# Performance work log

Measured on AMD Instinct MI355X. Metric: run time of the kernel, lower is better.

Reference implementation:

```python
import jax, jax.numpy as jnp
import numpy as np

D_FEAT = 6
T = 60
H = 64          # hidden_size
N = 8192        # number of stocks (cross-sectional batch)
LRELU_SLOPE = 0.01
BN_EPS = 1e-5


def _gru_layer(x_seq, W_ih, W_hh, b_ih, b_hh):
    """torch-convention GRU layer. x_seq: (N, T, in) -> (N, T, H)."""
    # precompute input projections for all timesteps: (N, T, 3H)
    xw = jnp.einsum('nti,gi->ntg', x_seq, W_ih) + b_ih

    def step(h, xt):
        gh = h @ W_hh.T + b_hh
        xr, xz, xn = jnp.split(xt, 3, axis=-1)
        hr, hz, hn = jnp.split(gh, 3, axis=-1)
        r = jax.nn.sigmoid(xr + hr)
        z = jax.nn.sigmoid(xz + hz)
        n = jnp.tanh(xn + r * hn)
        h_new = (1.0 - z) * n + z * h
        return h_new, h_new

    h0 = jnp.zeros((x_seq.shape[0], H), x_seq.dtype)
    _, ys = jax.lax.scan(step, h0, jnp.swapaxes(xw, 0, 1))  # (T, N, H)
    return jnp.swapaxes(ys, 0, 1)


def _batchnorm(x, w, b):
    # track_running_stats=False -> always batch statistics (biased var)
    m = jnp.mean(x, axis=0)
    v = jnp.var(x, axis=0)
    return (x - m) * jax.lax.rsqrt(v + BN_EPS) * w + b


def setup_inputs() -> dict:
    key = jax.random.key(0)
    ks = jax.random.split(key, 24)
    s = 1.0 / np.sqrt(H)

    def u(k, shape):
        return jax.random.uniform(k, shape, jnp.float32, -s, s)

    inp = {"x": jax.random.normal(ks[0], (N, D_FEAT * T), jnp.float32)}
    in_sizes = [D_FEAT, H]
    for l in range(2):
        inp[f"W_ih_l{l}"] = u(ks[1 + 4 * l], (3 * H, in_sizes[l]))
        inp[f"W_hh_l{l}"] = u(ks[2 + 4 * l], (3 * H, H))
        inp[f"b_ih_l{l}"] = u(ks[3 + 4 * l], (3 * H,))
        inp[f"b_hh_l{l}"] = u(ks[4 + 4 * l], (3 * H,))
    inp["bn1_w"] = 1.0 + 0.1 * jax.random.normal(ks[9], (H,), jnp.float32)
    inp["bn1_b"] = 0.1 * jax.random.normal(ks[10], (H,), jnp.float32)
    inp["fc_w"] = u(ks[11], (H, H))
    inp["fc_b"] = u(ks[12], (H,))
    inp["bn2_w"] = 1.0 + 0.1 * jax.random.normal(ks[13], (H,), jnp.float32)
    inp["bn2_b"] = 0.1 * jax.random.normal(ks[14], (H,), jnp.float32)
    inp["fc_out_w"] = u(ks[15], (1, H))
    inp["fc_out_b"] = u(ks[16], (1,))
    return inp


def reference(x, W_ih_l0, W_hh_l0, b_ih_l0, b_hh_l0,
              W_ih_l1, W_hh_l1, b_ih_l1, b_hh_l1,
              bn1_w, bn1_b, fc_w, fc_b, bn2_w, bn2_b, fc_out_w, fc_out_b):
    n = x.shape[0]
    xs = x.reshape(n, D_FEAT, -1).transpose(0, 2, 1)  # (N, T, d_feat)
    h = _gru_layer(xs, W_ih_l0, W_hh_l0, b_ih_l0, b_hh_l0)
    h = _gru_layer(h, W_ih_l1, W_hh_l1, b_ih_l1, b_hh_l1)
    hidden = h[:, -1, :]                               # (N, H)
    hidden = _batchnorm(hidden, bn1_w, bn1_b)

    # pairwise covariance: E[x_i * y_j] - E[x_i]E[y_j], mean over H.
    # Algebraically (x @ y.T)/H - e_x e_y^T; no O(N^2*H) intermediate.
    e = jnp.mean(hidden, axis=1, keepdims=True)        # (N, 1)
    gamma = hidden @ hidden.T / H - e @ e.T            # (N, N)

    out = gamma @ hidden                               # (N, H)
    out = out @ fc_w.T + fc_b
    out = _batchnorm(out, bn2_w, bn2_b)
    out = jnp.where(out >= 0, out, LRELU_SLOPE * out)  # LeakyReLU(0.01)
    return (out @ fc_out_w.T + fc_out_b).squeeze()
```

## Files before the change

kernel.cpp:

```cpp
#include <hip/hip_runtime.h>
#include <hip/hip_bf16.h>
#include <hip/hip_cooperative_groups.h>

namespace cg = cooperative_groups;

#define N_ROWS 8192
#define T_STEPS 60
#define DFEAT 6

typedef _Float16 f16x8 __attribute__((ext_vector_type(8)));
typedef float f32x4 __attribute__((ext_vector_type(4)));
typedef float fvec4 __attribute__((ext_vector_type(4)));

#if __has_builtin(__builtin_amdgcn_exp2f)
#define EXP2F(x) __builtin_amdgcn_exp2f(x)
#else
#define EXP2F(x) exp2f(x)
#endif
#define RCPF(x) __builtin_amdgcn_rcpf(x)

#define LOG2E  1.4426950408889634f
#define LOG2E2 2.8853900817779268f

#define MFMA16(a, b, c) __builtin_amdgcn_mfma_f32_16x16x32_f16(a, b, c, 0, 0, 0)

#define LOAD_WS(W, g, kf, SC, DST) do {                                       \
    const float* _p = (W) + ((g)*64 + jcol)*64 + (kf)*32 + rowgrp*8;          \
    fvec4 _v0 = *(const fvec4*)_p;                                            \
    fvec4 _v1 = *(const fvec4*)(_p + 4);                                      \
    f16x8 _f;                                                                 \
    _Pragma("unroll")                                                         \
    for (int _e = 0; _e < 4; ++_e) {                                          \
        _f[_e]     = (_Float16)(_v0[_e] * (SC));                              \
        _f[4 + _e] = (_Float16)(_v1[_e] * (SC));                              \
    }                                                                         \
    DST = _f;                                                                 \
} while (0)

__device__ __forceinline__ int hswz(int row, int col) {
    return row * 64 + (col ^ ((row & 7) << 3));
}

__global__ __launch_bounds__(512, 4)
void gru_fused(const float* __restrict__ x,
               const float* __restrict__ Wih0, const float* __restrict__ Whh0,
               const float* __restrict__ bih0, const float* __restrict__ bhh0,
               const float* __restrict__ Wih1, const float* __restrict__ Whh1,
               const float* __restrict__ bih1, const float* __restrict__ bhh1,
               float* __restrict__ hidden)
{
    __shared__ __align__(16) _Float16 h0s[2][1024];
    __shared__ __align__(16) _Float16 h1s[2][1024];
    __shared__ __align__(16) _Float16 xs[T_STEPS][16][8];
    __shared__ __align__(16) _Float16 zx[8];

    const int tid = threadIdx.x;
    const int lane = tid & 63;
    const int wv = tid >> 6;
    const int roleB = wv >> 2;
    const int cg_ = wv & 3;
    const int lrow = lane & 15;
    const int rowgrp = lane >> 4;
    const int jcol = cg_ * 16 + lrow;
    const int rbase = blockIdx.x * 16;

    for (int i = tid; i < 1024; i += 512) {
        h0s[0][i] = (_Float16)0.f; h0s[1][i] = (_Float16)0.f;
        h1s[0][i] = (_Float16)0.f; h1s[1][i] = (_Float16)0.f;
    }
    if (tid < 8) zx[tid] = (_Float16)0.f;
    for (int idx = tid; idx < 16 * T_STEPS; idx += 512) {
        int t = idx >> 4, r = idx & 15;
        const float* xp = x + (long)(rbase + r) * (DFEAT * T_STEPS) + t;
        f16x8 f;
#pragma unroll
        for (int d = 0; d < DFEAT; ++d) f[d] = (_Float16)xp[d * T_STEPS];
        f[6] = (_Float16)0.f; f[7] = (_Float16)0.f;
        *(f16x8*)&xs[t][r][0] = f;
    }

    f16x8 zerof;
#pragma unroll
    for (int e = 0; e < 8; ++e) zerof[e] = (_Float16)0.f;

    f16x8 wg[12];
#pragma unroll
    for (int i = 0; i < 12; ++i) wg[i] = zerof;
    float br, bz, bxn, bhn;
    if (roleB == 0) {
        LOAD_WS(Whh0, 0, 0, LOG2E,  wg[0]);  LOAD_WS(Whh0, 0, 1, LOG2E,  wg[1]);
        LOAD_WS(Whh0, 1, 0, LOG2E,  wg[2]);  LOAD_WS(Whh0, 1, 1, LOG2E,  wg[3]);
        LOAD_WS(Whh0, 2, 0, LOG2E2, wg[4]);  LOAD_WS(Whh0, 2, 1, LOG2E2, wg[5]);
        if (rowgrp == 0) {
#pragma unroll
            for (int g = 0; g < 3; ++g) {
                const float sc = (g == 2) ? LOG2E2 : LOG2E;
                f16x8 f = zerof;
#pragma unroll
                for (int e = 0; e < DFEAT; ++e)
                    f[e] = (_Float16)(Wih0[(g * 64 + jcol) * DFEAT + e] * sc);
                wg[6 + g] = f;
            }
        }
        br  = (bih0[jcol] + bhh0[jcol]) * LOG2E;
        bz  = (bih0[64 + jcol] + bhh0[64 + jcol]) * LOG2E;
        bxn = bih0[128 + jcol] * LOG2E2;
        bhn = bhh0[128 + jcol] * LOG2E2;
    } else {
        LOAD_WS(Wih1, 0, 0, LOG2E,  wg[0]);  LOAD_WS(Wih1, 0, 1, LOG2E,  wg[1]);
        LOAD_WS(Wih1, 1, 0, LOG2E,  wg[2]);  LOAD_WS(Wih1, 1, 1, LOG2E,  wg[3]);
        LOAD_WS(Wih1, 2, 0, LOG2E2, wg[4]);  LOAD_WS(Wih1, 2, 1, LOG2E2, wg[5]);
        LOAD_WS(Whh1, 0, 0, LOG2E,  wg[6]);  LOAD_WS(Whh1, 0, 1, LOG2E,  wg[7]);
        LOAD_WS(Whh1, 1, 0, LOG2E,  wg[8]);  LOAD_WS(Whh1, 1, 1, LOG2E,  wg[9]);
        LOAD_WS(Whh1, 2, 0, LOG2E2, wg[10]); LOAD_WS(Whh1, 2, 1, LOG2E2, wg[11]);
        br  = (bih1[jcol] + bhh1[jcol]) * LOG2E;
        bz  = (bih1[64 + jcol] + bhh1[64 + jcol]) * LOG2E;
        bxn = bih1[128 + jcol] * LOG2E2;
        bhn = bhh1[128 + jcol] * LOG2E2;
    }

    float hreg[4] = {0.f, 0.f, 0.f, 0.f};

    const _Float16* xbase_l = (rowgrp == 0) ? &xs[0][lrow][0] : &zx[0];
    const long xinc = (rowgrp == 0) ? 128 : 0;

    int widx[4];
#pragma unroll
    for (int q = 0; q < 4; ++q) widx[q] = hswz(rowgrp * 4 + q, jcol);
    const int ridx0 = lrow * 64 + ((rowgrp * 8) ^ ((lrow & 7) << 3));
    const int ridx1 = lrow * 64 + ((32 + rowgrp * 8) ^ ((lrow & 7) << 3));

    __syncthreads();

#pragma unroll 1
    for (int tt = 0; tt <= T_STEPS; ++tt) {
        if (roleB == 0) {
            if (tt < T_STEPS) {
                const int rb = (tt + 1) & 1;
                f16x8 hf0 = *(const f16x8*)&h0s[rb][ridx0];
                f16x8 hf1 = *(const f16x8*)&h0s[rb][ridx1];
                f16x8 xf  = *(const f16x8*)(xbase_l + (long)tt * xinc);
                f32x4 accr  = {br, br, br, br};
                f32x4 accz  = {bz, bz, bz, bz};
                f32x4 accxn = {bxn, bxn, bxn, bxn};
                f32x4 acchn = {bhn, bhn, bhn, bhn};
                accr  = MFMA16(xf,  wg[6], accr);
                accr  = MFMA16(hf0, wg[0], accr);
                accr  = MFMA16(hf1, wg[1], accr);
                accz  = MFMA16(xf,  wg[7], accz);
                accz  = MFMA16(hf0, wg[2], accz);
                accz  = MFMA16(hf1, wg[3], accz);
                accxn = MFMA16(xf,  wg[8], accxn);
                acchn = MFMA16(hf0, wg[4], acchn);
                acchn = MFMA16(hf1, wg[5], acchn);
#pragma unroll
                for (int q = 0; q < 4; ++q) {
                    float r = RCPF(1.0f + EXP2F(-accr[q]));
                    float z = RCPF(1.0f + EXP2F(-accz[q]));
                    float v = accxn[q] + r * acchn[q];
                    float n = 2.0f * RCPF(1.0f + EXP2F(-v)) - 1.0f;
                    hreg[q] = n + z * (hreg[q] - n);
                }
                const int wb = tt & 1;
#pragma unroll
                for (int q = 0; q < 4; ++q)
                    h0s[wb][widx[q]] = (_Float16)hreg[q];
            }
        } else {
            if (tt > 0) {
                const int rb0 = (tt + 1) & 1;
                const int rb1 = tt & 1;
                f16x8 xf0 = *(const f16x8*)&h0s[rb0][ridx0];
                f16x8 xf1 = *(const f16x8*)&h0s[rb0][ridx1];
                f16x8 hf0 = *(const f16x8*)&h1s[rb1][ridx0];
                f16x8 hf1 = *(const f16x8*)&h1s[rb1][ridx1];
                f32x4 accr  = {br, br, br, br};
                f32x4 accz  = {bz, bz, bz, bz};
                f32x4 accxn = {bxn, bxn, bxn, bxn};
                f32x4 acchn = {bhn, bhn, bhn, bhn};
                accr  = MFMA16(xf0, wg[0], accr);
                accr  = MFMA16(xf1, wg[1], accr);
                accr  = MFMA16(hf0, wg[6], accr);
                accr  = MFMA16(hf1, wg[7], accr);
                accz  = MFMA16(xf0, wg[2], accz);
                accz  = MFMA16(xf1, wg[3], accz);
                accz  = MFMA16(hf0, wg[8], accz);
                accz  = MFMA16(hf1, wg[9], accz);
                accxn = MFMA16(xf0, wg[4], accxn);
                accxn = MFMA16(xf1, wg[5], accxn);
                acchn = MFMA16(hf0, wg[10], acchn);
                acchn = MFMA16(hf1, wg[11], acchn);
#pragma unroll
                for (int q = 0; q < 4; ++q) {
                    float r = RCPF(1.0f + EXP2F(-accr[q]));
                    float z = RCPF(1.0f + EXP2F(-accz[q]));
                    float v = accxn[q] + r * acchn[q];
                    float n = 2.0f * RCPF(1.0f + EXP2F(-v)) - 1.0f;
                    hreg[q] = n + z * (hreg[q] - n);
                }
                const int wb = (tt + 1) & 1;
#pragma unroll
                for (int q = 0; q < 4; ++q)
                    h1s[wb][widx[q]] = (_Float16)hreg[q];
            }
        }
        __syncthreads();
    }

    if (roleB == 1) {
#pragma unroll
        for (int q = 0; q < 4; ++q)
            hidden[(long)(rbase + rowgrp * 4 + q) * 64 + jcol] = hreg[q];
    }
}

__global__ __launch_bounds__(256, 1)
void tail_kernel(const float* __restrict__ hidden,
                 const float* __restrict__ bn1w, const float* __restrict__ bn1b,
                 const float* __restrict__ fcw,  const float* __restrict__ fcb,
                 const float* __restrict__ bn2w, const float* __restrict__ bn2b,
                 const float* __restrict__ fow,  const float* __restrict__ fob,
                 float* __restrict__ y, float* wsb)
{
    float* csp    = wsb;
    float* cqp    = wsb + 4096;
    float* spart  = wsb + 8192;
    float* e2part = wsb + 12288;
    float* sred   = wsb + 12352;
    float* E2g    = wsb + 12416;
    float* Ag     = wsb + 12480;
    float* Bg     = wsb + 12544;
    float* bMg    = wsb + 12608;
    float* svg    = wsb + 12672;
    float* Mg     = wsb + 12736;
    float* Gpart  = wsb + 16832;

    __shared__ float tile[128][65];
    __shared__ float el[128];
    __shared__ float Fs[64][65];
    __shared__ float Msh[64][65];
    __shared__ float a1s[64], c1s[64], a2s[64], c2s[64];
    __shared__ float svs[64], fcs[64], wos[64];
    __shared__ float Grow[64];
    __shared__ float r4a[4][64], r4b[4][64];

    const int b = blockIdx.x, tid = threadIdx.x;
    cg::grid_group grid = cg::this_grid();

    for (int i = tid; i < 8192; i += 256)
        tile[i >> 6][i & 63] = hidden[b * 8192 + i];
    for (int i = tid; i < 4096; i += 256)
        Fs[i >> 6][i & 63] = fcw[i];
    __syncthreads();
    {
        const int c = tid & 63, g = tid >> 6;
        float s = 0.f, q = 0.f;
        for (int r = g * 32; r < g * 32 + 32; ++r) {
            float v = tile[r][c]; s += v; q += v * v;
        }
        r4a[g][c] = s; r4b[g][c] = q;
    }
    __syncthreads();
    if (tid < 64) {
        csp[b * 64 + tid] = r4a[0][tid] + r4a[1][tid] + r4a[2][tid] + r4a[3][tid];
        cqp[b * 64 + tid] = r4b[0][tid] + r4b[1][tid] + r4b[2][tid] + r4b[3][tid];
    }
    __threadfence();
    grid.sync();

    if (tid < 64) {
        float s = 0.f, q = 0.f;
        for (int bb = 0; bb < 64; ++bb) { s += csp[bb * 64 + tid]; q += cqp[bb * 64 + tid]; }
        float m = s * (1.0f / N_ROWS);
        float v = q * (1.0f / N_ROWS) - m * m;
        float a = bn1w[tid] * rsqrtf(v + 1e-5f);
        a1s[tid] = a; c1s[tid] = bn1b[tid] - m * a;
    }
    __syncthreads();
    for (int i = tid; i < 8192; i += 256) {
        int r = i >> 6, c = i & 63;
        tile[r][c] = tile[r][c] * a1s[c] + c1s[c];
    }
    __syncthreads();
    for (int r = tid; r < 128; r += 256) {
        float s = 0.f;
#pragma unroll 8
        for (int c = 0; c < 64; ++c) s += tile[r][c];
        el[r] = s * (1.0f / 64.0f);
    }
    __syncthreads();
    {
        const int j = tid & 63, kg = tid >> 6;
        float accG[16];
#pragma unroll
        for (int q = 0; q < 16; ++q) accG[q] = 0.f;
        for (int r = 0; r < 128; ++r) {
            float hj = tile[r][j];
#pragma unroll
            for (int q = 0; q < 16; ++q) accG[q] += tile[r][kg * 16 + q] * hj;
        }
#pragma unroll
        for (int q = 0; q < 16; ++q)
            Gpart[(b * 64 + kg * 16 + q) * 64 + j] = accG[q];
    }
    if (tid < 64) {
        float accS = 0.f;
        for (int r = 0; r < 128; ++r) accS += el[r] * tile[r][tid];
        spart[b * 64 + tid] = accS;
        float p = el[tid] * el[tid] + el[tid + 64] * el[tid + 64];
#pragma unroll
        for (int o = 32; o > 0; o >>= 1) p += __shfl_down(p, o);
        if (tid == 0) e2part[b] = p;
    }
    __threadfence();
    grid.sync();

    {
        const int j = tid & 63, g = tid >> 6;
        float p = 0.f;
        for (int bb = g * 16; bb < g * 16 + 16; ++bb)
            p += Gpart[(bb * 64 + b) * 64 + j];
        r4a[g][j] = p;
    }
    __syncthreads();
    if (tid < 64)
        Grow[tid] = r4a[0][tid] + r4a[1][tid] + r4a[2][tid] + r4a[3][tid];
    __syncthreads();
    if (tid < 64) {
        const int p = tid;
        float acc = 0.f;
#pragma unroll 8
        for (int j = 0; j < 64; ++j) acc += Grow[j] * Fs[p][j];
        Mg[b * 64 + p] = acc * (1.0f / 64.0f);
    }
    if (b == 0 && tid < 64) {
        float s = 0.f;
        for (int bb = 0; bb < 64; ++bb) s += spart[bb * 64 + tid];
        sred[tid] = s;
    }
    if (b == 1 && tid < 64) { Ag[tid] = 0.f; Bg[tid] = 0.f; bMg[tid] = 0.f; }
    if (b == 2 && tid == 0) {
        float e = 0.f;
        for (int bb = 0; bb < 64; ++bb) e += e2part[bb];
        E2g[0] = e;
    }
    __threadfence();
    grid.sync();

    for (int i = tid; i < 4096; i += 256)
        Msh[i >> 6][i & 63] = Mg[i];
    __syncthreads();
    if (tid < 64) {
        const int p = tid;
        float gm = 0.f;
#pragma unroll 8
        for (int kk = 0; kk < 64; ++kk) gm += Grow[kk] * Msh[kk][p];
        float mkp = Msh[b][p];
        atomicAdd(&Ag[p],  mkp * gm);
        atomicAdd(&Bg[p],  sred[b] * mkp);
        atomicAdd(&bMg[p], bn1b[b] * mkp);
    }
    if (b == 0 && tid < 64) {
        const int p = tid;
        float sv = 0.f;
#pragma unroll 8
        for (int j = 0; j < 64; ++j) sv += sred[j] * Fs[p][j];
        svg[p] = sv;
    }
    __threadfence();
    grid.sync();

    if (tid < 64) {
        const int p = tid;
        float bsum = 0.f;
        for (int j = 0; j < 64; ++j) bsum += bn1b[j];
        float Esum = (float)N_ROWS * bsum * (1.0f / 64.0f);
        float svp = svg[p];
        float Su  = (float)N_ROWS * bMg[p] - Esum * svp;
        float Su2 = Ag[p] - 2.0f * svp * Bg[p] + E2g[0] * svp * svp;
        float f = fcb[p];
        float cs = Su + (float)N_ROWS * f;
        float cq = Su2 + 2.0f * f * Su + (float)N_ROWS * f * f;
        float m2 = cs * (1.0f / N_ROWS);
        float v2 = cq * (1.0f / N_ROWS) - m2 * m2;
        float a = bn2w[p] * rsqrtf(v2 + 1e-5f);
        a2s[p] = a; c2s[p] = bn2b[p] - m2 * a;
        svs[p] = svp; fcs[p] = f; wos[p] = fow[p];
    }
    __syncthreads();
    const float bo = fob[0];
#pragma unroll 1
    for (int pass = 0; pass < 4; ++pass) {
        const int row = pass * 32 + (tid >> 3);
        const int pg = (tid & 7) << 3;
        float acc[8];
#pragma unroll
        for (int i = 0; i < 8; ++i) acc[i] = 0.f;
#pragma unroll 4
        for (int k = 0; k < 64; ++k) {
            float hv = tile[row][k];
#pragma unroll
            for (int i = 0; i < 8; ++i) acc[i] += hv * Msh[k][pg + i];
        }
        const float ev = el[row];
        float part = 0.f;
#pragma unroll
        for (int i = 0; i < 8; ++i) {
            int p = pg + i;
            float v = acc[i] - ev * svs[p] + fcs[p];
            v = v * a2s[p] + c2s[p];
            v = (v >= 0.f) ? v : 0.01f * v;
            part += v * wos[p];
        }
        part += __shfl_xor(part, 1);
        part += __shfl_xor(part, 2);
        part += __shfl_xor(part, 4);
        if ((tid & 7) == 0) y[b * 128 + row] = part + bo;
    }
}

extern "C" void kernel_launch(void* const* d_in, const int* in_sizes, int n_in,
                              void* d_out, int out_size, void* d_ws, size_t ws_size,
                              hipStream_t stream)
{
    const float* x    = (const float*)d_in[0];
    const float* Wih0 = (const float*)d_in[1];
    const float* Whh0 = (const float*)d_in[2];
    const float* bih0 = (const float*)d_in[3];
    const float* bhh0 = (const float*)d_in[4];
    const float* Wih1 = (const float*)d_in[5];
    const float* Whh1 = (const float*)d_in[6];
    const float* bih1 = (const float*)d_in[7];
    const float* bhh1 = (const float*)d_in[8];
    const float* bn1w = (const float*)d_in[9];
    const float* bn1b = (const float*)d_in[10];
    const float* fcw  = (const float*)d_in[11];
    const float* fcb  = (const float*)d_in[12];
    const float* bn2w = (const float*)d_in[13];
    const float* bn2b = (const float*)d_in[14];
    const float* fow  = (const float*)d_in[15];
    const float* fob  = (const float*)d_in[16];
    float* y = (float*)d_out;

    float* ws = (float*)d_ws;
    float* hidden = ws;
    float* wsb    = ws + 524288;

    gru_fused<<<512, 512, 0, stream>>>(x, Wih0, Whh0, bih0, bhh0,
                                       Wih1, Whh1, bih1, bhh1, hidden);

    void* args[] = {(void*)&hidden, (void*)&bn1w, (void*)&bn1b, (void*)&fcw,
                    (void*)&fcb, (void*)&bn2w, (void*)&bn2b, (void*)&fow,
                    (void*)&fob, (void*)&y, (void*)&wsb};
    hipLaunchCooperativeKernel((void*)tail_kernel, dim3(64), dim3(256),
                               args, 0, stream);
}
```

Baseline: 282.7 us.

## Replace cooperative tail with MFMA Gram kernel and algebraic BN1 folding

```diff
diff --git a/kernel.cpp b/kernel.cpp
--- a/kernel.cpp
+++ b/kernel.cpp
@@ -1,8 +1,5 @@
 #include <hip/hip_runtime.h>
 #include <hip/hip_bf16.h>
-#include <hip/hip_cooperative_groups.h>
-
-namespace cg = cooperative_groups;
 
 #define N_ROWS 8192
 #define T_STEPS 60
@@ -47,7 +44,7 @@
                const float* __restrict__ bih0, const float* __restrict__ bhh0,
                const float* __restrict__ Wih1, const float* __restrict__ Whh1,
                const float* __restrict__ bih1, const float* __restrict__ bhh1,
-               float* __restrict__ hidden)
+               _Float16* __restrict__ hidden, _Float16* __restrict__ hiddenT)
 {
     __shared__ __align__(16) _Float16 h0s[2][1024];
     __shared__ __align__(16) _Float16 h1s[2][1024];
@@ -209,185 +206,187 @@
 
     if (roleB == 1) {
 #pragma unroll
+        for (int q = 0; q < 4; ++q) {
+            const int row = rbase + rowgrp * 4 + q;
+            _Float16 hv = (_Float16)hreg[q];
+            hidden[(long)row * 64 + jcol] = hv;
+            hiddenT[(long)jcol * N_ROWS + row] = hv;
+        }
+    }
+}
+
+__global__ __launch_bounds__(256)
+void gram_kernel(const _Float16* __restrict__ hiddenT,
+                 float* __restrict__ Graw, float* __restrict__ colsum)
+{
+    __shared__ float red[3][64][4];
+    const int tid = threadIdx.x;
+    const int wv = tid >> 6, lane = tid & 63;
+    const int lrow = lane & 15, rg = lane >> 4;
+    const int r = blockIdx.x >> 2, c = blockIdx.x & 3;
+
+    const _Float16* pb = hiddenT + (long)(c * 16 + lrow) * N_ROWS + wv * 2048 + rg * 8;
+    f32x4 acc[4];
+#pragma unroll
+    for (int i = 0; i < 4; ++i) acc[i] = (f32x4){0.f, 0.f, 0.f, 0.f};
+
+    if (r < 4) {
+        const _Float16* pa = hiddenT + (long)(r * 16 + lrow) * N_ROWS + wv * 2048 + rg * 8;
+#pragma unroll 4
+        for (int kf = 0; kf < 64; ++kf) {
+            f16x8 af = *(const f16x8*)(pa + kf * 32);
+            f16x8 bf = *(const f16x8*)(pb + kf * 32);
+            acc[kf & 3] = MFMA16(af, bf, acc[kf & 3]);
+        }
+    } else {
+        f16x8 af;
+#pragma unroll
+        for (int e = 0; e < 8; ++e) af[e] = (lrow == 0) ? (_Float16)1.f : (_Float16)0.f;
+#pragma unroll 4
+        for (int kf = 0; kf < 64; ++kf) {
+            f16x8 bf = *(const f16x8*)(pb + kf * 32);
+            acc[kf & 3] = MFMA16(af, bf, acc[kf & 3]);
+        }
+    }
+    f32x4 a0 = acc[0] + acc[1] + acc[2] + acc[3];
+
+    if (wv > 0) {
+#pragma unroll
+        for (int q = 0; q < 4; ++q) red[wv - 1][lane][q] = a0[q];
+    }
+    __syncthreads();
+    if (wv == 0) {
+#pragma unroll
         for (int q = 0; q < 4; ++q)
-            hidden[(long)(rbase + rowgrp * 4 + q) * 64 + jcol] = hreg[q];
+            a0[q] += red[0][lane][q] + red[1][lane][q] + red[2][lane][q];
+        if (r < 4) {
+#pragma unroll
+            for (int q = 0; q < 4; ++q)
+                Graw[(r * 16 + rg * 4 + q) * 64 + c * 16 + lrow] = a0[q];
+        } else if (rg == 0) {
+            colsum[c * 16 + lrow] = a0[0];
+        }
     }
 }
 
-__global__ __launch_bounds__(256, 1)
-void tail_kernel(const float* __restrict__ hidden,
-                 const float* __restrict__ bn1w, const float* __restrict__ bn1b,
-                 const float* __restrict__ fcw,  const float* __restrict__ fcb,
-                 const float* __restrict__ bn2w, const float* __restrict__ bn2b,
-                 const float* __restrict__ fow,  const float* __restrict__ fob,
-                 float* __restrict__ y, float* wsb)
+__global__ __launch_bounds__(256)
+void final_kernel(const _Float16* __restrict__ hidden,
+                  const float* __restrict__ Graw, const float* __restrict__ colsum,
+                  const float* __restrict__ bn1w, const float* __restrict__ bn1b,
+                  const float* __restrict__ fcw,  const float* __restrict__ fcb,
+                  const float* __restrict__ bn2w, const float* __restrict__ bn2b,
+                  const float* __restrict__ fow,  const float* __restrict__ fob,
+                  float* __restrict__ y)
 {
-    float* csp    = wsb;
-    float* cqp    = wsb + 4096;
-    float* spart  = wsb + 8192;
-    float* e2part = wsb + 12288;
-    float* sred   = wsb + 12352;
-    float* E2g    = wsb + 12416;
-    float* Ag     = wsb + 12480;
-    float* Bg     = wsb + 12544;
-    float* bMg    = wsb + 12608;
-    float* svg    = wsb + 12672;
-    float* Mg     = wsb + 12736;
-    float* Gpart  = wsb + 16832;
-
-    __shared__ float tile[128][65];
+    __shared__ float Gbn[64][65];
+    __shared__ float Ms[64][65];
+    __shared__ _Float16 tile[128][72];
     __shared__ float el[128];
-    __shared__ float Fs[64][65];
-    __shared__ float Msh[64][65];
-    __shared__ float a1s[64], c1s[64], a2s[64], c2s[64];
-    __shared__ float svs[64], fcs[64], wos[64];
-    __shared__ float Grow[64];
-    __shared__ float r4a[4][64], r4b[4][64];
+    __shared__ float a1s[64], c1s[64], S1s[64], S1bn[64], s_s[64];
+    __shared__ float svs[64], a2s[64], c2s[64], fcs[64], wos[64];
+    __shared__ float red[4][64];
+    __shared__ float E2s, Esums;
 
     const int b = blockIdx.x, tid = threadIdx.x;
-    cg::grid_group grid = cg::this_grid();
-
-    for (int i = tid; i < 8192; i += 256)
-        tile[i >> 6][i & 63] = hidden[b * 8192 + i];
-    for (int i = tid; i < 4096; i += 256)
-        Fs[i >> 6][i & 63] = fcw[i];
-    __syncthreads();
+    const float Nf = (float)N_ROWS;
+
+    if (tid < 64) {
+        float S1 = colsum[tid];
+        S1s[tid] = S1;
+        float m = S1 * (1.0f / Nf);
+        float var = Graw[tid * 65] * (1.0f / Nf) - m * m;
+        float a = bn1w[tid] * rsqrtf(var + 1e-5f);
+        float cc = bn1b[tid] - m * a;
+        a1s[tid] = a; c1s[tid] = cc;
+        S1bn[tid] = a * S1 + Nf * cc;
+    }
+    __syncthreads();
+
+    for (int i = tid; i < 4096; i += 256) {
+        int j = i >> 6, k = i & 63;
+        Gbn[j][k] = a1s[j] * a1s[k] * Graw[i]
+                  + a1s[j] * c1s[k] * S1s[j]
+                  + c1s[j] * a1s[k] * S1s[k]
+                  + Nf * c1s[j] * c1s[k];
+    }
+    __syncthreads();
+
     {
-        const int c = tid & 63, g = tid >> 6;
-        float s = 0.f, q = 0.f;
-        for (int r = g * 32; r < g * 32 + 32; ++r) {
-            float v = tile[r][c]; s += v; q += v * v;
-        }
-        r4a[g][c] = s; r4b[g][c] = q;
-    }
-    __syncthreads();
+        const int k = tid & 63, g = tid >> 6;
+        float p = 0.f;
+        for (int j = g * 16; j < g * 16 + 16; ++j) p += Gbn[j][k];
+        red[g][k] = p;
+    }
+    __syncthreads();
+    if (tid < 64)
+        s_s[tid] = (red[0][tid] + red[1][tid] + red[2][tid] + red[3][tid]) * (1.0f / 64.0f);
+    __syncthreads();
+    if (tid == 0) {
+        float e2 = 0.f, es = 0.f;
+        for (int k = 0; k < 64; ++k) { e2 += s_s[k]; es += S1bn[k]; }
+        E2s = e2 * (1.0f / 64.0f);
+        Esums = es * (1.0f / 64.0f);
+    }
+
+    for (int i = tid; i < 4096; i += 256) {
+        int k = i >> 6, p = i & 63;
+        float acc = 0.f;
+#pragma unroll 8
+        for (int j = 0; j < 64; ++j) acc += Gbn[k][j] * fcw[p * 64 + j];
+        Ms[k][p] = acc * (1.0f / 64.0f);
+    }
+    __syncthreads();
+
+    {
+        const int p = tid & 63, g = tid >> 6;
+        float pa = 0.f;
+        for (int j = g * 16; j < g * 16 + 16; ++j) {
+            float gm = 0.f;
+#pragma unroll 8
+            for (int k = 0; k < 64; ++k) gm += Gbn[j][k] * Ms[k][p];
+            pa += Ms[j][p] * gm;
+        }
+        red[g][p] = pa;
+    }
+    __syncthreads();
+
     if (tid < 64) {
-        csp[b * 64 + tid] = r4a[0][tid] + r4a[1][tid] + r4a[2][tid] + r4a[3][tid];
-        cqp[b * 64 + tid] = r4b[0][tid] + r4b[1][tid] + r4b[2][tid] + r4b[3][tid];
-    }
-    __threadfence();
-    grid.sync();
-
-    if (tid < 64) {
-        float s = 0.f, q = 0.f;
-        for (int bb = 0; bb < 64; ++bb) { s += csp[bb * 64 + tid]; q += cqp[bb * 64 + tid]; }
-        float m = s * (1.0f / N_ROWS);
-        float v = q * (1.0f / N_ROWS) - m * m;
-        float a = bn1w[tid] * rsqrtf(v + 1e-5f);
-        a1s[tid] = a; c1s[tid] = bn1b[tid] - m * a;
-    }
-    __syncthreads();
-    for (int i = tid; i < 8192; i += 256) {
-        int r = i >> 6, c = i & 63;
-        tile[r][c] = tile[r][c] * a1s[c] + c1s[c];
+        const int p = tid;
+        float A = red[0][p] + red[1][p] + red[2][p] + red[3][p];
+        float sv = 0.f, B = 0.f, SuS = 0.f;
+#pragma unroll 8
+        for (int j = 0; j < 64; ++j) {
+            sv  += s_s[j] * fcw[p * 64 + j];
+            B   += s_s[j] * Ms[j][p];
+            SuS += S1bn[j] * Ms[j][p];
+        }
+        float Su  = SuS - Esums * sv;
+        float Su2 = A - 2.0f * sv * B + E2s * sv * sv;
+        float f = fcb[p];
+        float cs = Su + Nf * f;
+        float cq = Su2 + 2.0f * f * Su + Nf * f * f;
+        float m2 = cs * (1.0f / Nf);
+        float v2 = cq * (1.0f / Nf) - m2 * m2;
+        float a = bn2w[p] * rsqrtf(v2 + 1e-5f);
+        a2s[p] = a; c2s[p] = bn2b[p] - m2 * a;
+        svs[p] = sv; fcs[p] = f; wos[p] = fow[p];
+    }
+    __syncthreads();
+
+    for (int i = tid; i < 128 * 64; i += 256) {
+        int r = i >> 6, cc = i & 63;
+        float hv = (float)hidden[(long)(b * 128 + r) * 64 + cc];
+        tile[r][cc] = (_Float16)(hv * a1s[cc] + c1s[cc]);
     }
     __syncthreads();
     for (int r = tid; r < 128; r += 256) {
         float s = 0.f;
 #pragma unroll 8
-        for (int c = 0; c < 64; ++c) s += tile[r][c];
+        for (int cc = 0; cc < 64; ++cc) s += (float)tile[r][cc];
         el[r] = s * (1.0f / 64.0f);
     }
     __syncthreads();
-    {
-        const int j = tid & 63, kg = tid >> 6;
-        float accG[16];
-#pragma unroll
-        for (int q = 0; q < 16; ++q) accG[q] = 0.f;
-        for (int r = 0; r < 128; ++r) {
-            float hj = tile[r][j];
-#pragma unroll
-            for (int q = 0; q < 16; ++q) accG[q] += tile[r][kg * 16 + q] * hj;
-        }
-#pragma unroll
-        for (int q = 0; q < 16; ++q)
-            Gpart[(b * 64 + kg * 16 + q) * 64 + j] = accG[q];
-    }
-    if (tid < 64) {
-        float accS = 0.f;
-        for (int r = 0; r < 128; ++r) accS += el[r] * tile[r][tid];
-        spart[b * 64 + tid] = accS;
-        float p = el[tid] * el[tid] + el[tid + 64] * el[tid + 64];
-#pragma unroll
-        for (int o = 32; o > 0; o >>= 1) p += __shfl_down(p, o);
-        if (tid == 0) e2part[b] = p;
-    }
-    __threadfence();
-    grid.sync();
-
-    {
-        const int j = tid & 63, g = tid >> 6;
-        float p = 0.f;
-        for (int bb = g * 16; bb < g * 16 + 16; ++bb)
-            p += Gpart[(bb * 64 + b) * 64 + j];
-        r4a[g][j] = p;
-    }
-    __syncthreads();
-    if (tid < 64)
-        Grow[tid] = r4a[0][tid] + r4a[1][tid] + r4a[2][tid] + r4a[3][tid];
-    __syncthreads();
-    if (tid < 64) {
-        const int p = tid;
-        float acc = 0.f;
-#pragma unroll 8
-        for (int j = 0; j < 64; ++j) acc += Grow[j] * Fs[p][j];
-        Mg[b * 64 + p] = acc * (1.0f / 64.0f);
-    }
-    if (b == 0 && tid < 64) {
-        float s = 0.f;
-        for (int bb = 0; bb < 64; ++bb) s += spart[bb * 64 + tid];
-        sred[tid] = s;
-    }
-    if (b == 1 && tid < 64) { Ag[tid] = 0.f; Bg[tid] = 0.f; bMg[tid] = 0.f; }
-    if (b == 2 && tid == 0) {
-        float e = 0.f;
-        for (int bb = 0; bb < 64; ++bb) e += e2part[bb];
-        E2g[0] = e;
-    }
-    __threadfence();
-    grid.sync();
-
-    for (int i = tid; i < 4096; i += 256)
-        Msh[i >> 6][i & 63] = Mg[i];
-    __syncthreads();
-    if (tid < 64) {
-        const int p = tid;
-        float gm = 0.f;
-#pragma unroll 8
-        for (int kk = 0; kk < 64; ++kk) gm += Grow[kk] * Msh[kk][p];
-        float mkp = Msh[b][p];
-        atomicAdd(&Ag[p],  mkp * gm);
-        atomicAdd(&Bg[p],  sred[b] * mkp);
-        atomicAdd(&bMg[p], bn1b[b] * mkp);
-    }
-    if (b == 0 && tid < 64) {
-        const int p = tid;
-        float sv = 0.f;
-#pragma unroll 8
-        for (int j = 0; j < 64; ++j) sv += sred[j] * Fs[p][j];
-        svg[p] = sv;
-    }
-    __threadfence();
-    grid.sync();
-
-    if (tid < 64) {
-        const int p = tid;
-        float bsum = 0.f;
-        for (int j = 0; j < 64; ++j) bsum += bn1b[j];
-        float Esum = (float)N_ROWS * bsum * (1.0f / 64.0f);
-        float svp = svg[p];
-        float Su  = (float)N_ROWS * bMg[p] - Esum * svp;
-        float Su2 = Ag[p] - 2.0f * svp * Bg[p] + E2g[0] * svp * svp;
-        float f = fcb[p];
-        float cs = Su + (float)N_ROWS * f;
-        float cq = Su2 + 2.0f * f * Su + (float)N_ROWS * f * f;
-        float m2 = cs * (1.0f / N_ROWS);
-        float v2 = cq * (1.0f / N_ROWS) - m2 * m2;
-        float a = bn2w[p] * rsqrtf(v2 + 1e-5f);
-        a2s[p] = a; c2s[p] = bn2b[p] - m2 * a;
-        svs[p] = svp; fcs[p] = f; wos[p] = fow[p];
-    }
-    __syncthreads();
+
     const float bo = fob[0];
 #pragma unroll 1
     for (int pass = 0; pass < 4; ++pass) {
@@ -398,9 +397,9 @@
         for (int i = 0; i < 8; ++i) acc[i] = 0.f;
 #pragma unroll 4
         for (int k = 0; k < 64; ++k) {
-            float hv = tile[row][k];
-#pragma unroll
-            for (int i = 0; i < 8; ++i) acc[i] += hv * Msh[k][pg + i];
+            float hv = (float)tile[row][k];
+#pragma unroll
+            for (int i = 0; i < 8; ++i) acc[i] += hv * Ms[k][pg + i];
         }
         const float ev = el[row];
         float part = 0.f;
@@ -442,16 +441,15 @@
     const float* fob  = (const float*)d_in[16];
     float* y = (float*)d_out;
 
-    float* ws = (float*)d_ws;
-    float* hidden = ws;
-    float* wsb    = ws + 524288;
+    _Float16* hidden  = (_Float16*)d_ws;
+    _Float16* hiddenT = hidden + 524288;
+    float* Graw   = (float*)(hidden + 1048576);
+    float* colsum = Graw + 4096;
 
     gru_fused<<<512, 512, 0, stream>>>(x, Wih0, Whh0, bih0, bhh0,
-                                       Wih1, Whh1, bih1, bhh1, hidden);
-
-    void* args[] = {(void*)&hidden, (void*)&bn1w, (void*)&bn1b, (void*)&fcw,
-                    (void*)&fcb, (void*)&bn2w, (void*)&bn2b, (void*)&fow,
-                    (void*)&fob, (void*)&y, (void*)&wsb};
-    hipLaunchCooperativeKernel((void*)tail_kernel, dim3(64), dim3(256),
-                               args, 0, stream);
+                                       Wih1, Whh1, bih1, bhh1,
+                                       hidden, hiddenT);
+    gram_kernel<<<24, 256, 0, stream>>>(hiddenT, Graw, colsum);
+    final_kernel<<<64, 256, 0, stream>>>(hidden, Graw, colsum, bn1w, bn1b,
+                                         fcw, fcb, bn2w, bn2b, fow, fob, y);
 }
```

Result: faster. 232.5 us (-17.8%).
